# Optimization experiments

Hardware: AMD Instinct MI355X
Metric: run time of the kernel (lower is better)

The kernel has to match this reference:

```python
import jax, jax.numpy as jnp
import numpy as np

T, B = 256, 512
IMG_FLAT = 25          # 5*5*num_channels
FEAT = 16; LOC = 4; EMB = 4
LSTM_IN = FEAT + LOC + EMB  # 24
H = 128
GRID = 10.0


def _lin(k, out_d, in_d, scale=0.05):
    kw, kb = jax.random.split(k)
    return (jax.random.normal(kw, (out_d, in_d), jnp.float32) * scale,
            jax.random.normal(kb, (out_d,), jnp.float32) * scale)


def setup_inputs() -> dict:
    key = jax.random.key(0)
    ks = jax.random.split(key, 16)
    image = jax.random.uniform(ks[0], (T * B, 5, 5), jnp.float32) * 255.0
    location = jax.random.uniform(ks[1], (T * B, 2), jnp.float32) * GRID
    message = jax.random.normal(ks[2], (T * B, 1), jnp.float32)
    done = jax.random.randint(ks[3], (T * B,), 0, 2, jnp.int32)
    h0 = jnp.zeros((1, B, H), jnp.float32)
    c0 = jnp.zeros((1, B, H), jnp.float32)
    Wv1, bv1 = _lin(ks[4], 256, IMG_FLAT)
    Wv2, bv2 = _lin(ks[5], 256, 256)
    Wv3, bv3 = _lin(ks[6], 128, 256)
    Wv4, bv4 = _lin(ks[7], FEAT, 128)
    Wl, bl = _lin(ks[8], LOC, 2)
    Wm, bm = _lin(ks[9], EMB, 1)
    Wih, bih = _lin(ks[10], 4 * H, LSTM_IN)
    Whh, bhh = _lin(ks[11], 4 * H, H)
    return dict(image=image, location=location, message=message, done=done,
                h0=h0, c0=c0,
                Wv1=Wv1, bv1=bv1, Wv2=Wv2, bv2=bv2, Wv3=Wv3, bv3=bv3,
                Wv4=Wv4, bv4=bv4, Wl=Wl, bl=bl, Wm=Wm, bm=bm,
                Wih=Wih, bih=bih, Whh=Whh, bhh=bhh)


def _get_states(image, location, message, done_f, h0, c0,
                Wv1, bv1, Wv2, bv2, Wv3, bv3, Wv4, bv4,
                Wl, bl, Wm, bm, Wih, bih, Whh, bhh):
    batch = h0.shape[1]
    # encoders (all rows at once, faithful to torch version)
    x = image.reshape(image.shape[0], -1) / 255.0
    f = jax.nn.relu(x @ Wv1.T + bv1)
    f = jax.nn.relu(f @ Wv2.T + bv2)
    f = jax.nn.relu(f @ Wv3.T + bv3)
    image_feat = jax.nn.relu(f @ Wv4.T + bv4)                  # [TB, 16]
    loc_feat = (location / GRID) @ Wl.T + bl                    # [TB, 4]
    msg = (1.0 - done_f)[:, None] * message
    msg_feat = jax.nn.relu(msg @ Wm.T + bm)                     # [TB, 4]
    hid = jnp.concatenate([image_feat, loc_feat, msg_feat], axis=1)
    hid = hid.reshape(-1, batch, LSTM_IN)                       # [T, B, 24]
    d_seq = done_f.reshape(-1, batch)                           # [T, B]

    def step(carry, xd):
        h, c = carry
        x_t, d_t = xd
        mask = (1.0 - d_t)[:, None]
        h = h * mask
        c = c * mask
        gates = x_t @ Wih.T + bih + h @ Whh.T + bhh             # [B, 4H]
        i, fg, g, o = jnp.split(gates, 4, axis=-1)
        c = jax.nn.sigmoid(fg) * c + jax.nn.sigmoid(i) * jnp.tanh(g)
        h = jax.nn.sigmoid(o) * jnp.tanh(c)
        return (h, c), h

    (hT, cT), hs = jax.lax.scan(step, (h0[0], c0[0]), (hid, d_seq))
    new_hidden = hs.reshape(-1, H)                              # [TB, 128]
    return new_hidden, hT[None], cT[None]


def reference(image, location, message, done, h0, c0,
              Wv1, bv1, Wv2, bv2, Wv3, bv3, Wv4, bv4,
              Wl, bl, Wm, bm, Wih, bih, Whh, bhh):
    done_f = done.astype(jnp.float32)
    return _get_states(image, location, message, done_f, h0, c0,
                       Wv1, bv1, Wv2, bv2, Wv3, bv3, Wv4, bv4,
                       Wl, bl, Wm, bm, Wih, bih, Whh, bhh)
```

## Files before the change

### kernel.cpp

```cpp
#include <hip/hip_runtime.h>
#include <hip/hip_bf16.h>

#define T_STEPS 256
#define BATCH   512
#define HID     128
#define TBROWS  (T_STEPS * BATCH)
#define XH_STRIDE 32

typedef short  bh8   __attribute__((ext_vector_type(8)));
typedef _Float16 h8  __attribute__((ext_vector_type(8)));
typedef float  f32x4 __attribute__((ext_vector_type(4)));

__device__ __forceinline__ unsigned short f2bf_bits(float x) {
    union { float f; unsigned int u; } a; a.f = x;
    unsigned int r = a.u + 0x7fffu + ((a.u >> 16) & 1u);
    return (unsigned short)(r >> 16);
}
__device__ __forceinline__ unsigned short f2h_bits(float x) {
    union { _Float16 h; unsigned short u; } z; z.h = (_Float16)x; return z.u;
}
__device__ __forceinline__ unsigned int pack2h(float a, float b) {
    union { _Float16 h[2]; unsigned int u; } z;
    z.h[0] = (_Float16)a; z.h[1] = (_Float16)b; return z.u;
}
__device__ __forceinline__ unsigned int pack2bf(float a, float b) {
    return (unsigned int)f2bf_bits(a) | ((unsigned int)f2bf_bits(b) << 16);
}

#if __has_builtin(__builtin_amdgcn_rcpf)
__device__ __forceinline__ float frcp(float x) { return __builtin_amdgcn_rcpf(x); }
#else
__device__ __forceinline__ float frcp(float x) { return 1.0f / x; }
#endif
#if __has_builtin(__builtin_amdgcn_exp2f)
__device__ __forceinline__ float fexp2(float x) { return __builtin_amdgcn_exp2f(x); }
#else
__device__ __forceinline__ float fexp2(float x) { return __expf(x * 0.6931471806f); }
#endif
#define LOG2E 1.442695041f
__device__ __forceinline__ float sigf(float x) {
    return frcp(1.0f + fexp2(-x * LOG2E));
}
__device__ __forceinline__ float tanh_fast(float x) {
    return fmaf(-2.0f, frcp(1.0f + fexp2(x * (2.0f * LOG2E))), 1.0f);
}

__device__ __forceinline__ float swz16(float v) {
    return __int_as_float(
        __builtin_amdgcn_ds_swizzle(__float_as_int(v), 0x000F));
}

__device__ __forceinline__ void barrier_lds_only() {
    asm volatile("s_waitcnt lgkmcnt(0)" ::: "memory");
    __builtin_amdgcn_s_barrier();
    asm volatile("" ::: "memory");
}

__device__ __forceinline__ void fragstore(unsigned short* dst, const float* W,
                                          int i, int NT, int Kreal) {
    const int j    = i & 7;
    const int lane = (i >> 3) & 63;
    const int ts   = i >> 9;
    const int nt   = ts % NT;
    const int ks   = ts / NT;
    const int n = nt * 16 + (lane & 15);
    const int k = ks * 32 + (lane >> 4) * 8 + j;
    dst[i] = (k < Kreal) ? f2bf_bits(W[n * Kreal + k]) : (unsigned short)0;
}

#define NE1 8192
#define NE2 65536
#define NE3 32768
#define NE4 2048
#define NWC 81920
#define NBS 512
#define PREP_TOTAL (NE1 + NE2 + NE3 + NE4 + NWC + NBS)

__global__ __launch_bounds__(256) void prep_kernel(
    const float* __restrict__ W1, const float* __restrict__ W2,
    const float* __restrict__ W3, const float* __restrict__ W4,
    const float* __restrict__ Wih, const float* __restrict__ bih,
    const float* __restrict__ Whh, const float* __restrict__ bhh,
    unsigned short* __restrict__ w1f, unsigned short* __restrict__ w2f,
    unsigned short* __restrict__ w3f, unsigned short* __restrict__ w4f,
    unsigned short* __restrict__ wcf, float* __restrict__ bsum)
{
    int i = blockIdx.x * 256 + threadIdx.x;
    if (i < NE1) { fragstore(w1f, W1, i, 16, 25); return; }
    i -= NE1;
    if (i < NE2) { fragstore(w2f, W2, i, 16, 256); return; }
    i -= NE2;
    if (i < NE3) { fragstore(w3f, W3, i, 8, 256); return; }
    i -= NE3;
    if (i < NE4) { fragstore(w4f, W4, i, 1, 128); return; }
    i -= NE4;
    if (i < NWC) {
        const int j    = i & 7;
        const int lane = (i >> 3) & 63;
        const int ts   = i >> 9;
        const int mt   = ts / 5;
        const int kt   = ts - mt * 5;
        const int m = mt * 16 + (lane & 15);
        const int k = kt * 32 + (lane >> 4) * 8 + j;
        float v = 0.0f;
        if (k < 128)      v = Whh[m * 128 + k];
        else if (k < 152) v = Wih[m * 24 + (k - 128)];
        wcf[i] = f2h_bits(v);
        return;
    }
    i -= NWC;
    if (i < NBS) bsum[i] = bih[i] + bhh[i];
}

#define ASTRIDE 264

__global__ __launch_bounds__(256) void encoder_kernel(
    const float* __restrict__ img,
    const float* __restrict__ loc,
    const float* __restrict__ msg,
    const int*   __restrict__ done,
    const float* __restrict__ B1, const float* __restrict__ B2,
    const float* __restrict__ B3, const float* __restrict__ B4,
    const float* __restrict__ Wl, const float* __restrict__ Bl,
    const float* __restrict__ Wm, const float* __restrict__ Bm,
    const unsigned short* __restrict__ w1f, const unsigned short* __restrict__ w2f,
    const unsigned short* __restrict__ w3f, const unsigned short* __restrict__ w4f,
    unsigned short* __restrict__ xcat_h)
{
    __shared__ __align__(16) unsigned short actA[4][32][ASTRIDE];
    __shared__ __align__(16) unsigned short actB[4][32][ASTRIDE];

    const int tid  = threadIdx.x;
    const int w    = tid >> 6;
    const int lane = tid & 63;
    const int n    = lane & 15;
    const int quad = lane >> 4;
    const int wrow0 = blockIdx.x * 128 + w * 32;

    if (tid < 128) {
        const int grow = blockIdx.x * 128 + tid;
        const float l0 = loc[(size_t)grow * 2 + 0] * 0.1f;
        const float l1 = loc[(size_t)grow * 2 + 1] * 0.1f;
        #pragma unroll
        for (int c = 0; c < 4; ++c)
            xcat_h[(size_t)grow * XH_STRIDE + 16 + c] =
                f2h_bits(fmaf(Wl[c * 2 + 0], l0, fmaf(Wl[c * 2 + 1], l1, Bl[c])));
        const float mm = (1.0f - (float)done[grow]) * msg[grow];
        #pragma unroll
        for (int c = 0; c < 4; ++c)
            xcat_h[(size_t)grow * XH_STRIDE + 20 + c] =
                f2h_bits(fmaxf(fmaf(Wm[c], mm, Bm[c]), 0.0f));
    }

    const f32x4 zero4 = {0.0f, 0.0f, 0.0f, 0.0f};

    {
        bh8 bimg[2];
        #pragma unroll
        for (int sg = 0; sg < 2; ++sg) {
            const size_t grow = wrow0 + sg * 16 + n;
            #pragma unroll
            for (int j = 0; j < 8; ++j) {
                const int k = quad * 8 + j;
                const float v = (k < 25) ? img[grow * 25 + k] * (1.0f / 255.0f) : 0.0f;
                bimg[sg][j] = (short)f2bf_bits(v);
            }
        }
        f32x4 a1[16][2];
        #pragma unroll
        for (int mt = 0; mt < 16; ++mt) {
            const bh8 a = *reinterpret_cast<const bh8*>(w1f + (size_t)(mt * 64 + lane) * 8);
            a1[mt][0] = __builtin_amdgcn_mfma_f32_16x16x32_bf16(a, bimg[0], zero4, 0, 0, 0);
            a1[mt][1] = __builtin_amdgcn_mfma_f32_16x16x32_bf16(a, bimg[1], zero4, 0, 0, 0);
        }
        #pragma unroll
        for (int mt = 0; mt < 16; ++mt) {
            const float4 bv = *reinterpret_cast<const float4*>(B1 + mt * 16 + quad * 4);
            #pragma unroll
            for (int sg = 0; sg < 2; ++sg) {
                const float v0 = fmaxf(a1[mt][sg][0] + bv.x, 0.0f);
                const float v1 = fmaxf(a1[mt][sg][1] + bv.y, 0.0f);
                const float v2 = fmaxf(a1[mt][sg][2] + bv.z, 0.0f);
                const float v3 = fmaxf(a1[mt][sg][3] + bv.w, 0.0f);
                uint2 pk; pk.x = pack2bf(v0, v1); pk.y = pack2bf(v2, v3);
                *reinterpret_cast<uint2*>(&actA[w][sg * 16 + n][mt * 16 + quad * 4]) = pk;
            }
        }
    }
    __syncthreads();

    {
        f32x4 a2[16][2];
        #pragma unroll
        for (int mt = 0; mt < 16; ++mt) { a2[mt][0] = zero4; a2[mt][1] = zero4; }
        #pragma unroll
        for (int kt = 0; kt < 8; ++kt) {
            const bh8 b0 = *reinterpret_cast<const bh8*>(&actA[w][n][kt * 32 + quad * 8]);
            const bh8 b1 = *reinterpret_cast<const bh8*>(&actA[w][16 + n][kt * 32 + quad * 8]);
            #pragma unroll
            for (int mt = 0; mt < 16; ++mt) {
                const bh8 a = *reinterpret_cast<const bh8*>(
                    w2f + (size_t)((kt * 16 + mt) * 64 + lane) * 8);
                a2[mt][0] = __builtin_amdgcn_mfma_f32_16x16x32_bf16(a, b0, a2[mt][0], 0, 0, 0);
                a2[mt][1] = __builtin_amdgcn_mfma_f32_16x16x32_bf16(a, b1, a2[mt][1], 0, 0, 0);
            }
        }
        #pragma unroll
        for (int mt = 0; mt < 16; ++mt) {
            const float4 bv = *reinterpret_cast<const float4*>(B2 + mt * 16 + quad * 4);
            #pragma unroll
            for (int sg = 0; sg < 2; ++sg) {
                const float v0 = fmaxf(a2[mt][sg][0] + bv.x, 0.0f);
                const float v1 = fmaxf(a2[mt][sg][1] + bv.y, 0.0f);
                const float v2 = fmaxf(a2[mt][sg][2] + bv.z, 0.0f);
                const float v3 = fmaxf(a2[mt][sg][3] + bv.w, 0.0f);
                uint2 pk; pk.x = pack2bf(v0, v1); pk.y = pack2bf(v2, v3);
                *reinterpret_cast<uint2*>(&actB[w][sg * 16 + n][mt * 16 + quad * 4]) = pk;
            }
        }
    }
    __syncthreads();

    {
        f32x4 a3[8][2];
        #pragma unroll
        for (int mt = 0; mt < 8; ++mt) { a3[mt][0] = zero4; a3[mt][1] = zero4; }
        #pragma unroll
        for (int kt = 0; kt < 8; ++kt) {
            const bh8 b0 = *reinterpret_cast<const bh8*>(&actB[w][n][kt * 32 + quad * 8]);
            const bh8 b1 = *reinterpret_cast<const bh8*>(&actB[w][16 + n][kt * 32 + quad * 8]);
            #pragma unroll
            for (int mt = 0; mt < 8; ++mt) {
                const bh8 a = *reinterpret_cast<const bh8*>(
                    w3f + (size_t)((kt * 8 + mt) * 64 + lane) * 8);
                a3[mt][0] = __builtin_amdgcn_mfma_f32_16x16x32_bf16(a, b0, a3[mt][0], 0, 0, 0);
                a3[mt][1] = __builtin_amdgcn_mfma_f32_16x16x32_bf16(a, b1, a3[mt][1], 0, 0, 0);
            }
        }
        #pragma unroll
        for (int mt = 0; mt < 8; ++mt) {
            const float4 bv = *reinterpret_cast<const float4*>(B3 + mt * 16 + quad * 4);
            #pragma unroll
            for (int sg = 0; sg < 2; ++sg) {
                const float v0 = fmaxf(a3[mt][sg][0] + bv.x, 0.0f);
                const float v1 = fmaxf(a3[mt][sg][1] + bv.y, 0.0f);
                const float v2 = fmaxf(a3[mt][sg][2] + bv.z, 0.0f);
                const float v3 = fmaxf(a3[mt][sg][3] + bv.w, 0.0f);
                uint2 pk; pk.x = pack2bf(v0, v1); pk.y = pack2bf(v2, v3);
                *reinterpret_cast<uint2*>(&actA[w][sg * 16 + n][mt * 16 + quad * 4]) = pk;
            }
        }
    }
    __syncthreads();

    {
        f32x4 a4[2] = {zero4, zero4};
        #pragma unroll
        for (int kt = 0; kt < 4; ++kt) {
            const bh8 b0 = *reinterpret_cast<const bh8*>(&actA[w][n][kt * 32 + quad * 8]);
            const bh8 b1 = *reinterpret_cast<const bh8*>(&actA[w][16 + n][kt * 32 + quad * 8]);
            const bh8 a = *reinterpret_cast<const bh8*>(w4f + (size_t)(kt * 64 + lane) * 8);
            a4[0] = __builtin_amdgcn_mfma_f32_16x16x32_bf16(a, b0, a4[0], 0, 0, 0);
            a4[1] = __builtin_amdgcn_mfma_f32_16x16x32_bf16(a, b1, a4[1], 0, 0, 0);
        }
        const float4 bv = *reinterpret_cast<const float4*>(B4 + quad * 4);
        #pragma unroll
        for (int sg = 0; sg < 2; ++sg) {
            const int grow = wrow0 + sg * 16 + n;
            const float v0 = fmaxf(a4[sg][0] + bv.x, 0.0f);
            const float v1 = fmaxf(a4[sg][1] + bv.y, 0.0f);
            const float v2 = fmaxf(a4[sg][2] + bv.z, 0.0f);
            const float v3 = fmaxf(a4[sg][3] + bv.w, 0.0f);
            uint2 pk; pk.x = pack2h(v0, v1); pk.y = pack2h(v2, v3);
            *reinterpret_cast<uint2*>(xcat_h + (size_t)grow * XH_STRIDE + quad * 4) = pk;
        }
    }
}

#define COLS 2
#define HXS 168

__global__ __launch_bounds__(512) void lstm_kernel(
    const unsigned short* __restrict__ xcat_h,
    const int*   __restrict__ done,
    const float* __restrict__ h0,
    const float* __restrict__ c0,
    const unsigned short* __restrict__ wcf,
    const float* __restrict__ bsum,
    float* __restrict__ out)
{
    __shared__ __align__(16) unsigned short hx[2][COLS][HXS];

    const int tid  = threadIdx.x;
    const int w    = tid >> 6;
    const int lane = tid & 63;
    const int n    = lane & 15;
    const int quad = lane >> 4;
    const int bb   = blockIdx.x * COLS;

    h8 wf[4][5];
    #pragma unroll
    for (int g = 0; g < 4; ++g)
        #pragma unroll
        for (int kt = 0; kt < 5; ++kt)
            wf[g][kt] = *reinterpret_cast<const h8*>(
                wcf + (size_t)(((g * 8 + w) * 5 + kt) * 64 + lane) * 8);

    const int unit = w * 16 + n;
    f32x4 bini[4];
    #pragma unroll
    for (int g = 0; g < 4; ++g) {
        const float b = bsum[g * 128 + unit];
        bini[g] = (f32x4){b, b, b, b};
    }

    const bool owner = (lane < 32);
    const int col = quad & 1;

    float c_ = 0.0f, h0v = 0.0f;
    if (owner) {
        c_  = c0[(size_t)(bb + col) * HID + unit];
        h0v = h0[(size_t)(bb + col) * HID + unit];
    }

    for (int i = tid; i < 2 * COLS * HXS / 2; i += 512)
        reinterpret_cast<unsigned int*>(hx)[i] = 0u;
    __syncthreads();

    int mc = 0, mn = 0;
    if (owner) {
        mc = done[bb + col];
        mn = done[BATCH + bb + col];
        hx[0][col][unit] = f2h_bits(h0v * (1.0f - (float)mc));
    }
    if (tid < COLS * 12) {
        const int nl = tid / 12, kp = tid - nl * 12;
        *reinterpret_cast<unsigned int*>(&hx[0][nl][128 + 2 * kp]) =
            *reinterpret_cast<const unsigned int*>(
                xcat_h + (size_t)(bb + nl) * XH_STRIDE + 2 * kp);
    }
    __syncthreads();

    float hl = 0.0f;

    h8 bf[5];
    #pragma unroll
    for (int kt = 0; kt < 5; ++kt) bf[kt] = (h8)(_Float16)0.0f;

    #pragma unroll 1
    for (int s = 0; s < T_STEPS; ++s) {
        const int buf = s & 1;

        if (n < COLS) {
            #pragma unroll
            for (int kt = 0; kt < 5; ++kt)
                bf[kt] = *reinterpret_cast<const h8*>(&hx[buf][n][kt * 32 + quad * 8]);
        }

        unsigned int xreg = 0;
        if (tid < COLS * 12) {
            const int nl = tid / 12, kp = tid - nl * 12;
            const int rowx = (s + 1 < T_STEPS ? s + 1 : T_STEPS - 1) * BATCH + bb + nl;
            xreg = *reinterpret_cast<const unsigned int*>(
                xcat_h + (size_t)rowx * XH_STRIDE + 2 * kp);
        }
        const int mf = done[(s + 2 < T_STEPS ? s + 2 : T_STEPS - 1) * BATCH + bb + col];

        f32x4 acc[4];
        #pragma unroll
        for (int g = 0; g < 4; ++g) acc[g] = bini[g];
        #pragma unroll
        for (int kt = 0; kt < 5; ++kt)
            #pragma unroll
            for (int g = 0; g < 4; ++g)
                acc[g] = __builtin_amdgcn_mfma_f32_16x16x32_f16(
                    bf[kt], wf[g][kt], acc[g], 0, 0, 0);

        float g4[4];
        #pragma unroll
        for (int g = 0; g < 4; ++g) {
            const float t0 = swz16(acc[g][0]);
            const float t1 = swz16(acc[g][1]);
            g4[g] = (lane & 16) ? t1 : t0;
        }

        if (owner) {
            const float cn = sigf(g4[1]) * (c_ * (1.0f - (float)mc))
                           + sigf(g4[0]) * tanh_fast(g4[2]);
            const float hn = sigf(g4[3]) * tanh_fast(cn);
            c_ = cn; hl = hn;
            out[(size_t)(s * BATCH + bb + col) * HID + unit] = hn;
            hx[buf ^ 1][col][unit] = f2h_bits(hn * (1.0f - (float)mn));
            mc = mn; mn = mf;
        }
        if (tid < COLS * 12) {
            const int nl = tid / 12, kp = tid - nl * 12;
            *reinterpret_cast<unsigned int*>(&hx[buf ^ 1][nl][128 + 2 * kp]) = xreg;
        }
        barrier_lds_only();
    }

    const size_t base = (size_t)TBROWS * HID;
    if (owner) {
        out[base + (size_t)(bb + col) * HID + unit] = hl;
        out[base + (size_t)BATCH * HID + (size_t)(bb + col) * HID + unit] = c_;
    }
}

extern "C" void kernel_launch(void* const* d_in, const int* in_sizes, int n_in,
                              void* d_out, int out_size, void* d_ws, size_t ws_size,
                              hipStream_t stream) {
    const float* img  = (const float*)d_in[0];
    const float* loc  = (const float*)d_in[1];
    const float* msg  = (const float*)d_in[2];
    const int*   done = (const int*)d_in[3];
    const float* h0   = (const float*)d_in[4];
    const float* c0   = (const float*)d_in[5];
    const float* W1   = (const float*)d_in[6];
    const float* B1   = (const float*)d_in[7];
    const float* W2   = (const float*)d_in[8];
    const float* B2   = (const float*)d_in[9];
    const float* W3   = (const float*)d_in[10];
    const float* B3   = (const float*)d_in[11];
    const float* W4   = (const float*)d_in[12];
    const float* B4   = (const float*)d_in[13];
    const float* Wl   = (const float*)d_in[14];
    const float* Bl   = (const float*)d_in[15];
    const float* Wm   = (const float*)d_in[16];
    const float* Bm   = (const float*)d_in[17];
    const float* Wih  = (const float*)d_in[18];
    const float* bih  = (const float*)d_in[19];
    const float* Whh  = (const float*)d_in[20];
    const float* bhh  = (const float*)d_in[21];

    char* wsb = (char*)d_ws;
    unsigned short* xcat_h = (unsigned short*)wsb;
    unsigned short* w1f = (unsigned short*)(wsb + (size_t)TBROWS * XH_STRIDE * 2);
    unsigned short* w2f = w1f + NE1;
    unsigned short* w3f = w2f + NE2;
    unsigned short* w4f = w3f + NE3;
    unsigned short* wcf = w4f + NE4;
    float*          bsum = (float*)(wcf + NWC);

    float* out = (float*)d_out;

    prep_kernel<<<(PREP_TOTAL + 255) / 256, 256, 0, stream>>>(
        W1, W2, W3, W4, Wih, bih, Whh, bhh,
        w1f, w2f, w3f, w4f, wcf, bsum);
    encoder_kernel<<<TBROWS / 128, 256, 0, stream>>>(
        img, loc, msg, done, B1, B2, B3, B4, Wl, Bl, Wm, Bm,
        w1f, w2f, w3f, w4f, xcat_h);
    lstm_kernel<<<BATCH / COLS, 512, 0, stream>>>(
        xcat_h, done, h0, c0, wcf, bsum, out);
}
```

Before: 378.2 us.

## Preload per-block LSTM inputs and done masks into LDS before recurrence

Before the time loop, each block copies its full sequence of projected inputs (all 256 steps for its 2 columns) and done flags into shared memory. Inside the serial recurrence, the per-step global loads of the next x row and future done flags are replaced by LDS reads, and the x staging into the hidden buffer is removed. This takes global-memory latency out of the latency-bound step loop. In exchange it adds an upfront bulk load and about 34 KB of LDS per block, which could limit occupancy.

```diff
diff --git a/kernel.cpp b/kernel.cpp
--- a/kernel.cpp
+++ b/kernel.cpp
@@ -278,7 +278,6 @@
 }
 
 #define COLS 2
-#define HXS 168
 
 __global__ __launch_bounds__(512) void lstm_kernel(
     const unsigned short* __restrict__ xcat_h,
@@ -289,7 +288,9 @@
     const float* __restrict__ bsum,
     float* __restrict__ out)
 {
-    __shared__ __align__(16) unsigned short hx[2][COLS][HXS];
+    __shared__ __align__(16) unsigned short xls[T_STEPS][COLS][32];
+    __shared__ __align__(16) unsigned short hx[2][COLS][HID];
+    __shared__ int dls[T_STEPS][COLS];
 
     const int tid  = threadIdx.x;
     const int w    = tid >> 6;
@@ -298,6 +299,21 @@
     const int quad = lane >> 4;
     const int bb   = blockIdx.x * COLS;
 
+    for (int i = tid; i < T_STEPS * COLS * 16; i += 512) {
+        const int dw = i & 15;
+        const int rc = i >> 4;
+        const int st = rc >> 1, cl = rc & 1;
+        unsigned int v = 0u;
+        if (dw < 12)
+            v = *reinterpret_cast<const unsigned int*>(
+                xcat_h + (size_t)(st * BATCH + bb + cl) * XH_STRIDE + dw * 2);
+        *reinterpret_cast<unsigned int*>(&xls[st][cl][dw * 2]) = v;
+    }
+    if (tid < T_STEPS * COLS) {
+        const int st = tid >> 1, cl = tid & 1;
+        dls[st][cl] = done[st * BATCH + bb + cl];
+    }
+
     h8 wf[4][5];
     #pragma unroll
     for (int g = 0; g < 4; ++g)
@@ -322,23 +338,10 @@
         c_  = c0[(size_t)(bb + col) * HID + unit];
         h0v = h0[(size_t)(bb + col) * HID + unit];
     }
-
-    for (int i = tid; i < 2 * COLS * HXS / 2; i += 512)
-        reinterpret_cast<unsigned int*>(hx)[i] = 0u;
     __syncthreads();
 
-    int mc = 0, mn = 0;
-    if (owner) {
-        mc = done[bb + col];
-        mn = done[BATCH + bb + col];
-        hx[0][col][unit] = f2h_bits(h0v * (1.0f - (float)mc));
-    }
-    if (tid < COLS * 12) {
-        const int nl = tid / 12, kp = tid - nl * 12;
-        *reinterpret_cast<unsigned int*>(&hx[0][nl][128 + 2 * kp]) =
-            *reinterpret_cast<const unsigned int*>(
-                xcat_h + (size_t)(bb + nl) * XH_STRIDE + 2 * kp);
-    }
+    if (owner)
+        hx[0][col][unit] = f2h_bits(h0v * (1.0f - (float)dls[0][col]));
     __syncthreads();
 
     float hl = 0.0f;
@@ -353,18 +356,14 @@
 
         if (n < COLS) {
             #pragma unroll
-            for (int kt = 0; kt < 5; ++kt)
+            for (int kt = 0; kt < 4; ++kt)
                 bf[kt] = *reinterpret_cast<const h8*>(&hx[buf][n][kt * 32 + quad * 8]);
-        }
-
-        unsigned int xreg = 0;
-        if (tid < COLS * 12) {
-            const int nl = tid / 12, kp = tid - nl * 12;
-            const int rowx = (s + 1 < T_STEPS ? s + 1 : T_STEPS - 1) * BATCH + bb + nl;
-            xreg = *reinterpret_cast<const unsigned int*>(
-                xcat_h + (size_t)rowx * XH_STRIDE + 2 * kp);
-        }
-        const int mf = done[(s + 2 < T_STEPS ? s + 2 : T_STEPS - 1) * BATCH + bb + col];
+            bf[4] = *reinterpret_cast<const h8*>(&xls[s][n][quad * 8]);
+        }
+
+        const int sn = (s + 1 < T_STEPS) ? s + 1 : T_STEPS - 1;
+        const int m_cur = dls[s][col];
+        const int m_nxt = dls[sn][col];
 
         f32x4 acc[4];
         #pragma unroll
@@ -385,17 +384,12 @@
         }
 
         if (owner) {
-            const float cn = sigf(g4[1]) * (c_ * (1.0f - (float)mc))
+            const float cn = sigf(g4[1]) * (c_ * (1.0f - (float)m_cur))
                            + sigf(g4[0]) * tanh_fast(g4[2]);
             const float hn = sigf(g4[3]) * tanh_fast(cn);
             c_ = cn; hl = hn;
             out[(size_t)(s * BATCH + bb + col) * HID + unit] = hn;
-            hx[buf ^ 1][col][unit] = f2h_bits(hn * (1.0f - (float)mn));
-            mc = mn; mn = mf;
-        }
-        if (tid < COLS * 12) {
-            const int nl = tid / 12, kp = tid - nl * 12;
-            *reinterpret_cast<unsigned int*>(&hx[buf ^ 1][nl][128 + 2 * kp]) = xreg;
+            hx[buf ^ 1][col][unit] = f2h_bits(hn * (1.0f - (float)m_nxt));
         }
         barrier_lds_only();
     }
```

Result: no change. 378.1 us (-0.0%).
